# Kernel tuning notes

Measured on AMD Instinct MI355X. Metric: run time of the kernel, lower is better.

## Reference

```python
import jax, jax.numpy as jnp
import numpy as np

B, S, D, H = 4, 2048, 1024, 16
DH = D // H  # 64


def setup_inputs() -> dict:
    key = jax.random.key(0)
    ks = jax.random.split(key, 11)
    s = 0.02
    return {
        "query": jax.random.normal(ks[0], (B, S, D), jnp.float32),
        "key": jax.random.normal(ks[1], (B, S, D), jnp.float32),
        "value": jax.random.normal(ks[2], (B, S, D), jnp.float32),
        "Wq": jax.random.normal(ks[3], (D, D), jnp.float32) * s,
        "bq": jnp.zeros((D,), jnp.float32),
        "Wk": jax.random.normal(ks[4], (D, D), jnp.float32) * s,
        "bk": jnp.zeros((D,), jnp.float32),
        "Wv": jax.random.normal(ks[5], (D, D), jnp.float32) * s,
        "bv": jnp.zeros((D,), jnp.float32),
        "Wo": jax.random.normal(ks[6], (D, D), jnp.float32) * s,
        "bo": jnp.zeros((D,), jnp.float32),
    }


def reference(query, key, value, Wq, bq, Wk, bk, Wv, bv, Wo, bo):
    b, s, _ = query.shape
    # linear projections (torch Linear: x @ W^T + b; here W stored as [in, out])
    q = query @ Wq + bq
    k = key @ Wk + bk
    v = value @ Wv + bv
    # split heads -> [B, H, S, DH]
    q = q.reshape(b, s, H, DH).transpose(0, 2, 1, 3)
    k = k.reshape(b, s, H, DH).transpose(0, 2, 1, 3)
    v = v.reshape(b, s, H, DH).transpose(0, 2, 1, 3)
    scale = jnp.sqrt(jnp.asarray(DH, jnp.float32))
    attn = jnp.einsum("bhqd,bhkd->bhqk", q, k) / scale  # [B,H,S,S]
    attn = jax.nn.softmax(attn, axis=-1)
    out = jnp.einsum("bhqk,bhkd->bhqd", attn, v)
    out = out.transpose(0, 2, 1, 3).reshape(b, s, D)
    return out @ Wo + bo
```

## Files before the change

kernel.cpp:

```cpp
#include <hip/hip_runtime.h>

typedef float f32x4 __attribute__((ext_vector_type(4)));
typedef __bf16 bf16x8 __attribute__((ext_vector_type(8)));
typedef unsigned short u16;
typedef unsigned int u32;
typedef u16 u16x4 __attribute__((ext_vector_type(4)));
typedef u16 u16x8 __attribute__((ext_vector_type(8)));
typedef u32 u32x2 __attribute__((ext_vector_type(2)));
typedef u32 u32x4 __attribute__((ext_vector_type(4)));

constexpr int Bn = 4, Sn = 2048, Dn = 1024, Hn = 16, DHn = 64;
constexpr int Mn = Bn * Sn;

static __device__ __forceinline__ u16 f2bf(float f) {
  return __builtin_bit_cast(u16, (__bf16)f);
}

static __device__ __forceinline__ u32 cvtpk(float lo, float hi) {
  u32 r;
  asm("v_cvt_pk_bf16_f32 %0, %1, %2" : "=v"(r) : "v"(lo), "v"(hi));
  return r;
}

static __device__ __forceinline__ void async16(const void* g, void* l) {
  __builtin_amdgcn_global_load_lds((const __attribute__((address_space(1))) u32*)g,
                                   (__attribute__((address_space(3))) u32*)l, 16, 0, 0);
}

static __device__ __forceinline__ void wait_bar2() {
  asm volatile("s_waitcnt vmcnt(2)" ::: "memory");
  __builtin_amdgcn_sched_barrier(0);
  __builtin_amdgcn_s_barrier();
  __builtin_amdgcn_sched_barrier(0);
}
static __device__ __forceinline__ void wait_bar4() {
  asm volatile("s_waitcnt vmcnt(4)" ::: "memory");
  __builtin_amdgcn_sched_barrier(0);
  __builtin_amdgcn_s_barrier();
  __builtin_amdgcn_sched_barrier(0);
}
static __device__ __forceinline__ void wait_bar8() {
  asm volatile("s_waitcnt vmcnt(8)" ::: "memory");
  __builtin_amdgcn_sched_barrier(0);
  __builtin_amdgcn_s_barrier();
  __builtin_amdgcn_sched_barrier(0);
}
static __device__ __forceinline__ void wait_bar0() {
  asm volatile("s_waitcnt vmcnt(0)" ::: "memory");
  __builtin_amdgcn_sched_barrier(0);
  __builtin_amdgcn_s_barrier();
  __builtin_amdgcn_sched_barrier(0);
}
static __device__ __forceinline__ void raw_bar() {
  __builtin_amdgcn_sched_barrier(0);
  __builtin_amdgcn_s_barrier();
  __builtin_amdgcn_sched_barrier(0);
}
static __device__ __forceinline__ void lgkm_bar() {
  asm volatile("s_waitcnt lgkmcnt(0)" ::: "memory");
  __builtin_amdgcn_sched_barrier(0);
  __builtin_amdgcn_s_barrier();
  __builtin_amdgcn_sched_barrier(0);
}

__global__ void __launch_bounds__(256) transpose4_kernel(const float* __restrict__ Wq,
                                                         const float* __restrict__ Wk,
                                                         const float* __restrict__ Wv,
                                                         const float* __restrict__ Wo,
                                                         u16* __restrict__ Wts) {
  __shared__ float tile[32][33];
  const int z = blockIdx.z;
  const float* W = (z == 0) ? Wq : (z == 1) ? Wk : (z == 2) ? Wv : Wo;
  u16* Wt = Wts + (size_t)z * Dn * Dn;
  const int n0 = blockIdx.x * 32, k0 = blockIdx.y * 32;
  const int tx = threadIdx.x & 31, ty = (threadIdx.x >> 5) * 4;
#pragma unroll
  for (int i = 0; i < 4; ++i)
    tile[ty + i][tx] = W[(size_t)(k0 + ty + i) * Dn + n0 + tx];
  __syncthreads();
#pragma unroll
  for (int i = 0; i < 4; ++i)
    Wt[(size_t)(n0 + ty + i) * Dn + k0 + tx] = f2bf(tile[tx][ty + i]);
}

__global__ void __launch_bounds__(256) gemm_qkv_kernel(const float* __restrict__ q_in,
                                                       const float* __restrict__ k_in,
                                                       const float* __restrict__ v_in,
                                                       const u16* __restrict__ Wts,
                                                       const float* __restrict__ bq,
                                                       const float* __restrict__ bk,
                                                       const float* __restrict__ bv,
                                                       u16* __restrict__ outbase) {
  __shared__ u16 As[2][128 * 64];
  __shared__ u16 Bs[2][128 * 64];

  const int bid = blockIdx.x;
  const int xcd = bid & 7;
  const int loc = bid >> 3;
  const int nb = loc & 7;
  const int panel = xcd * 24 + (loc >> 3);
  const int z = panel >> 6;
  const int m0 = (panel & 63) * 128, n0 = nb * 128;

  const float* A = (z == 0) ? q_in : (z == 1) ? k_in : v_in;
  const u16* Bt = Wts + (size_t)z * Dn * Dn;
  const float* bias = (z == 0) ? bq : (z == 1) ? bk : bv;
  u16* outp = outbase + (size_t)z * Mn * Dn;
  const float scale = (z == 0) ? 0.125f * 1.4426950408889634f : 1.0f;

  const int tid = threadIdx.x;
  const int wave = tid >> 6, lane = tid & 63;
  const int g = lane >> 4, c = lane & 15;
  const int wm = wave >> 1, wn = wave & 1;
  const int srow = lane >> 3, blk = lane & 7;

  f32x4 acc[4][4] = {};
  constexpr int NK = Dn / 64;

  f32x4 ralo[4], rahi[4];

  auto issueA = [&](int k0) {
#pragma unroll
    for (int i = 0; i < 4; ++i) {
      const int row = (wave * 4 + i) * 8 + srow;
      const float* src = A + (size_t)(m0 + row) * Dn + k0 + blk * 8;
      ralo[i] = *(const f32x4*)src;
      rahi[i] = *(const f32x4*)(src + 4);
    }
  };
  auto writeA = [&](u16* dst) {
#pragma unroll
    for (int i = 0; i < 4; ++i) {
      const int row = (wave * 4 + i) * 8 + srow;
      u32x4 w;
      w[0] = cvtpk(ralo[i][0], ralo[i][1]);
      w[1] = cvtpk(ralo[i][2], ralo[i][3]);
      w[2] = cvtpk(rahi[i][0], rahi[i][1]);
      w[3] = cvtpk(rahi[i][2], rahi[i][3]);
      *(u32x4*)(dst + row * 64 + ((blk ^ srow) * 8)) = w;
    }
  };
  auto issueB = [&](int k0, u16* dstB) {
#pragma unroll
    for (int i = 0; i < 4; ++i) {
      const int ch = wave * 4 + i, row = ch * 8 + srow, sb = blk ^ srow;
      async16(Bt + (size_t)(n0 + row) * Dn + k0 + sb * 8, dstB + ch * 512);
    }
  };

  issueA(0);
  issueB(0, Bs[0]);
  asm volatile("s_waitcnt vmcnt(4)" ::: "memory");
  __builtin_amdgcn_sched_barrier(0);
  writeA(As[0]);
  issueA(64);
  issueB(64, Bs[1]);
  asm volatile("s_waitcnt lgkmcnt(0)" ::: "memory");
  __builtin_amdgcn_sched_barrier(0);

  for (int k = 0; k < NK; ++k) {
    const int cur = k & 1;
    if (k + 1 < NK) wait_bar4(); else wait_bar0();

    if (k + 1 < NK) writeA(As[cur ^ 1]);

#pragma unroll
    for (int kk = 0; kk < 2; ++kk) {
      bf16x8 af[4], bfr[4];
#pragma unroll
      for (int mi = 0; mi < 4; ++mi)
        af[mi] = *(const bf16x8*)(As[cur] + (wm * 64 + mi * 16 + c) * 64 +
                                  (((kk * 4 + g) ^ (c & 7)) * 8));
#pragma unroll
      for (int ni = 0; ni < 4; ++ni)
        bfr[ni] = *(const bf16x8*)(Bs[cur] + (wn * 64 + ni * 16 + c) * 64 +
                                   (((kk * 4 + g) ^ (c & 7)) * 8));
#pragma unroll
      for (int mi = 0; mi < 4; ++mi)
#pragma unroll
        for (int ni = 0; ni < 4; ++ni)
          acc[mi][ni] = __builtin_amdgcn_mfma_f32_16x16x32_bf16(af[mi], bfr[ni],
                                                                acc[mi][ni], 0, 0, 0);
    }

    lgkm_bar();
    if (k + 2 < NK) {
      issueA((k + 2) * 64);
      issueB((k + 2) * 64, Bs[cur]);
    }
  }

  const bool vmode = (z == 2);
#pragma unroll
  for (int ni = 0; ni < 4; ++ni) {
    const int col = n0 + wn * 64 + ni * 16 + c;
    const float bv = bias[col];
    const int hh = col >> 6, dh = col & 63;
#pragma unroll
    for (int mi = 0; mi < 4; ++mi) {
      const int row = m0 + wm * 64 + mi * 16 + g * 4;
      const int bb = row >> 11, s = row & 2047;
      if (!vmode) {
        u16* o = outp + (((size_t)(bb * Hn + hh) * Sn + s) * DHn + dh);
#pragma unroll
        for (int r = 0; r < 4; ++r)
          o[(size_t)r * DHn] = f2bf((acc[mi][ni][r] + bv) * scale);
      } else {
        u16x4 pk;
#pragma unroll
        for (int r = 0; r < 4; ++r) pk[r] = f2bf(acc[mi][ni][r] + bv);
        *(u16x4*)(outp + ((size_t)(bb * Hn + hh) * DHn + dh) * Sn + s) = pk;
      }
    }
  }
}

__global__ void __launch_bounds__(256) gemm_o_kernel(const u16* __restrict__ A,
                                                     const u16* __restrict__ Bt,
                                                     const float* __restrict__ bias,
                                                     float* __restrict__ outp) {
  __shared__ u16 As[2][128 * 64];
  __shared__ u16 Bs[2][128 * 64];
  const int bid = blockIdx.x;
  const int xcd = bid & 7;
  const int loc = bid >> 3;
  const int nb = loc & 7;
  const int panel = xcd * 8 + (loc >> 3);
  const int m0 = panel * 128, n0 = nb * 128;

  const int tid = threadIdx.x;
  const int wave = tid >> 6, lane = tid & 63;
  const int g = lane >> 4, c = lane & 15;
  const int wm = wave >> 1, wn = wave & 1;
  const int srow = lane >> 3, blk = lane & 7;

  f32x4 acc[4][4] = {};
  constexpr int NK = Dn / 64;

#pragma unroll
  for (int p = 0; p < 2; ++p) {
    const int k0 = p * 64;
#pragma unroll
    for (int i = 0; i < 4; ++i) {
      const int ch = wave * 4 + i;
      const int row = ch * 8 + srow;
      const int sblk = blk ^ srow;
      async16(A + (size_t)(m0 + row) * Dn + k0 + sblk * 8, As[p] + ch * 512);
      async16(Bt + (size_t)(n0 + row) * Dn + k0 + sblk * 8, Bs[p] + ch * 512);
    }
  }

  for (int k = 0; k < NK; ++k) {
    const int cur = k & 1;
    if (k + 1 < NK) wait_bar8(); else wait_bar0();

#pragma unroll
    for (int kk = 0; kk < 2; ++kk) {
      bf16x8 af[4], bfr[4];
#pragma unroll
      for (int mi = 0; mi < 4; ++mi)
        af[mi] = *(const bf16x8*)(As[cur] + (wm * 64 + mi * 16 + c) * 64 +
                                  (((kk * 4 + g) ^ (c & 7)) * 8));
#pragma unroll
      for (int ni = 0; ni < 4; ++ni)
        bfr[ni] = *(const bf16x8*)(Bs[cur] + (wn * 64 + ni * 16 + c) * 64 +
                                   (((kk * 4 + g) ^ (c & 7)) * 8));
#pragma unroll
      for (int mi = 0; mi < 4; ++mi)
#pragma unroll
        for (int ni = 0; ni < 4; ++ni)
          acc[mi][ni] = __builtin_amdgcn_mfma_f32_16x16x32_bf16(af[mi], bfr[ni],
                                                                acc[mi][ni], 0, 0, 0);
    }

    raw_bar();
    if (k + 2 < NK) {
      const int k0 = (k + 2) * 64;
#pragma unroll
      for (int i = 0; i < 4; ++i) {
        const int ch = wave * 4 + i;
        const int row = ch * 8 + srow;
        const int sblk = blk ^ srow;
        async16(A + (size_t)(m0 + row) * Dn + k0 + sblk * 8, As[cur] + ch * 512);
        async16(Bt + (size_t)(n0 + row) * Dn + k0 + sblk * 8, Bs[cur] + ch * 512);
      }
    }
  }

#pragma unroll
  for (int ni = 0; ni < 4; ++ni) {
    const int col = n0 + wn * 64 + ni * 16 + c;
    const float bv = bias[col];
#pragma unroll
    for (int mi = 0; mi < 4; ++mi) {
      const int row = m0 + wm * 64 + mi * 16 + g * 4;
      float* o = outp + (size_t)row * Dn + col;
#pragma unroll
      for (int r = 0; r < 4; ++r) o[(size_t)r * Dn] = acc[mi][ni][r] + bv;
    }
  }
}

__global__ void __launch_bounds__(512, 4) attn_kernel(const u16* __restrict__ Q,
                                                      const u16* __restrict__ Kp,
                                                      const u16* __restrict__ VT,
                                                      u16* __restrict__ O) {
  __shared__ u16 Ks[3][64 * 64];
  __shared__ u16 Vs[3][64 * 64];
  const int tid = threadIdx.x;
  const int wave = tid >> 6, lane = tid & 63;
  const int g = lane >> 4, c = lane & 15;
  const int bh = blockIdx.x;
  const int q0 = blockIdx.y * 256 + wave * 32;
  const u16* Qb = Q + (size_t)bh * Sn * DHn;
  const u16* Kb = Kp + (size_t)bh * Sn * DHn;
  const u16* Vb = VT + (size_t)bh * DHn * Sn;

  bf16x8 qf[2][2];
#pragma unroll
  for (int fq = 0; fq < 2; ++fq)
#pragma unroll
    for (int kk = 0; kk < 2; ++kk)
      qf[fq][kk] = *(const bf16x8*)(Qb + (size_t)(q0 + fq * 16 + c) * DHn + kk * 32 + g * 8);

  f32x4 ot[4][2] = {};
  f32x4 lacc[2] = {};
  u16x8 one8u;
#pragma unroll
  for (int j = 0; j < 8; ++j) one8u[j] = 0x3F80;
  const bf16x8 one8 = __builtin_bit_cast(bf16x8, one8u);
  const f32x4 zf = {};

  const int srow = lane >> 3, blk = lane & 7;
  const int krow = wave * 8 + srow;
  const int sblk = blk ^ srow;
  constexpr int NT = Sn / 64;

  u16 *kA = Ks[0], *kB = Ks[1], *kC = Ks[2];
  u16 *vA = Vs[0], *vB = Vs[1], *vC = Vs[2];

#pragma unroll
  for (int tt = 0; tt < 2; ++tt) {
    const int kt = tt * 64;
    async16(Kb + (size_t)(kt + krow) * DHn + sblk * 8, Ks[tt] + wave * 512);
    async16(Vb + (size_t)krow * Sn + kt + sblk * 8, Vs[tt] + wave * 512);
  }

  for (int t = 0; t < NT; ++t) {
    if (t + 1 < NT) wait_bar2(); else wait_bar0();

    if (t + 2 < NT) {
      const int kt = (t + 2) * 64;
      async16(Kb + (size_t)(kt + krow) * DHn + sblk * 8, kC + wave * 512);
      async16(Vb + (size_t)krow * Sn + kt + sblk * 8, vC + wave * 512);
    }

    f32x4 st[4][2];
    {
      bf16x8 kf[4];
#pragma unroll
      for (int fk = 0; fk < 4; ++fk)
        kf[fk] = *(const bf16x8*)(kA + (fk * 16 + c) * 64 + ((g ^ (c & 7)) * 8));
      __builtin_amdgcn_s_setprio(1);
#pragma unroll
      for (int fk = 0; fk < 4; ++fk)
#pragma unroll
        for (int fq = 0; fq < 2; ++fq)
          st[fk][fq] = __builtin_amdgcn_mfma_f32_16x16x32_bf16(kf[fk], qf[fq][0],
                                                               zf, 0, 0, 0);
      __builtin_amdgcn_s_setprio(0);
#pragma unroll
      for (int fk = 0; fk < 4; ++fk)
        kf[fk] = *(const bf16x8*)(kA + (fk * 16 + c) * 64 + (((4 + g) ^ (c & 7)) * 8));
      __builtin_amdgcn_s_setprio(1);
#pragma unroll
      for (int fk = 0; fk < 4; ++fk)
#pragma unroll
        for (int fq = 0; fq < 2; ++fq)
          st[fk][fq] = __builtin_amdgcn_mfma_f32_16x16x32_bf16(kf[fk], qf[fq][1],
                                                               st[fk][fq], 0, 0, 0);
      __builtin_amdgcn_s_setprio(0);
    }

#pragma unroll
    for (int fq = 0; fq < 2; ++fq)
#pragma unroll
      for (int fk = 0; fk < 4; ++fk)
#pragma unroll
        for (int r = 0; r < 4; ++r)
          st[fk][fq][r] = __builtin_amdgcn_exp2f(st[fk][fq][r]);

    bf16x8 pf[2][2];
#pragma unroll
    for (int fq = 0; fq < 2; ++fq)
#pragma unroll
      for (int kk = 0; kk < 2; ++kk) {
        u32x4 pw;
#pragma unroll
        for (int w = 0; w < 2; ++w) {
          const u32 a = cvtpk(st[2 * kk][fq][2 * w], st[2 * kk][fq][2 * w + 1]);
          const u32 b = cvtpk(st[2 * kk + 1][fq][2 * w], st[2 * kk + 1][fq][2 * w + 1]);
          const u32x2 p1 = __builtin_amdgcn_permlane32_swap(a, b, false, false);
          const u32x2 p2 = __builtin_amdgcn_permlane16_swap(p1[0], p1[1], false, false);
          pw[w] = p2[0];
          pw[2 + w] = p2[1];
        }
        pf[kk][fq] = __builtin_bit_cast(bf16x8, pw);
      }

#pragma unroll
    for (int kk = 0; kk < 2; ++kk) {
      bf16x8 vf[4];
#pragma unroll
      for (int fa = 0; fa < 4; ++fa)
        vf[fa] = *(const bf16x8*)(vA + (fa * 16 + c) * 64 +
                                  (((kk * 4 + g) ^ (c & 7)) * 8));
      __builtin_amdgcn_s_setprio(1);
#pragma unroll
      for (int fa = 0; fa < 4; ++fa)
#pragma unroll
        for (int fq = 0; fq < 2; ++fq)
          ot[fa][fq] = __builtin_amdgcn_mfma_f32_16x16x32_bf16(vf[fa], pf[kk][fq],
                                                               ot[fa][fq], 0, 0, 0);
#pragma unroll
      for (int fq = 0; fq < 2; ++fq)
        lacc[fq] = __builtin_amdgcn_mfma_f32_16x16x32_bf16(one8, pf[kk][fq],
                                                           lacc[fq], 0, 0, 0);
      __builtin_amdgcn_s_setprio(0);
    }

    u16* tk = kA; kA = kB; kB = kC; kC = tk;
    u16* tv = vA; vA = vB; vB = vC; vC = tv;
  }

  const int bb = bh >> 4, hh = bh & 15;
#pragma unroll
  for (int fq = 0; fq < 2; ++fq) {
    const float inv = 1.f / lacc[fq][0];
    const int s = q0 + fq * 16 + c;
#pragma unroll
    for (int fa = 0; fa < 4; ++fa) {
      const int dh = fa * 16 + g * 4;
      u16x4 pk;
#pragma unroll
      for (int r = 0; r < 4; ++r) pk[r] = f2bf(ot[fa][fq][r] * inv);
      *(u16x4*)(O + ((size_t)bb * Sn + s) * Dn + hh * 64 + dh) = pk;
    }
  }
}

extern "C" void kernel_launch(void* const* d_in, const int* in_sizes, int n_in,
                              void* d_out, int out_size, void* d_ws, size_t ws_size,
                              hipStream_t stream) {
  (void)in_sizes; (void)n_in; (void)out_size; (void)ws_size;
  const float* q_in = (const float*)d_in[0];
  const float* k_in = (const float*)d_in[1];
  const float* v_in = (const float*)d_in[2];
  const float* Wq = (const float*)d_in[3];
  const float* bq = (const float*)d_in[4];
  const float* Wk = (const float*)d_in[5];
  const float* bk = (const float*)d_in[6];
  const float* Wv = (const float*)d_in[7];
  const float* bv = (const float*)d_in[8];
  const float* Wo = (const float*)d_in[9];
  const float* bo = (const float*)d_in[10];

  char* ws = (char*)d_ws;
  const size_t szX = (size_t)Mn * Dn * 2;
  const size_t szW = (size_t)Dn * Dn * 2;
  u16* Wts = (u16*)ws;
  u16* Qb = (u16*)(ws + 4 * szW + 0 * szX);
  u16* Kb = (u16*)(ws + 4 * szW + 1 * szX);
  u16* VTb = (u16*)(ws + 4 * szW + 2 * szX);
  u16* Ob = (u16*)(ws + 4 * szW + 3 * szX);

  transpose4_kernel<<<dim3(32, 32, 4), 256, 0, stream>>>(Wq, Wk, Wv, Wo, Wts);

  gemm_qkv_kernel<<<1536, 256, 0, stream>>>(q_in, k_in, v_in, Wts, bq, bk, bv, Qb);

  attn_kernel<<<dim3(Bn * Hn, Sn / 256), 512, 0, stream>>>(Qb, Kb, VTb, Ob);

  gemm_o_kernel<<<512, 256, 0, stream>>>(Ob, Wts + (size_t)3 * Dn * Dn, bo,
                                         (float*)d_out);
}
```

Before: 180.9 us.

## Pre-convert QKV inputs to bf16 and async-load A tiles into LDS

```diff
diff --git a/kernel.cpp b/kernel.cpp
--- a/kernel.cpp
+++ b/kernel.cpp
@@ -33,12 +33,6 @@
   __builtin_amdgcn_s_barrier();
   __builtin_amdgcn_sched_barrier(0);
 }
-static __device__ __forceinline__ void wait_bar4() {
-  asm volatile("s_waitcnt vmcnt(4)" ::: "memory");
-  __builtin_amdgcn_sched_barrier(0);
-  __builtin_amdgcn_s_barrier();
-  __builtin_amdgcn_sched_barrier(0);
-}
 static __device__ __forceinline__ void wait_bar8() {
   asm volatile("s_waitcnt vmcnt(8)" ::: "memory");
   __builtin_amdgcn_sched_barrier(0);
@@ -56,11 +50,21 @@
   __builtin_amdgcn_s_barrier();
   __builtin_amdgcn_sched_barrier(0);
 }
-static __device__ __forceinline__ void lgkm_bar() {
-  asm volatile("s_waitcnt lgkmcnt(0)" ::: "memory");
-  __builtin_amdgcn_sched_barrier(0);
-  __builtin_amdgcn_s_barrier();
-  __builtin_amdgcn_sched_barrier(0);
+
+__global__ void __launch_bounds__(256) cvt3_kernel(const float* __restrict__ q,
+                                                   const float* __restrict__ k,
+                                                   const float* __restrict__ v,
+                                                   u16* __restrict__ dst) {
+  const int i = blockIdx.x * 256 + threadIdx.x;
+  const int t = i >> 20;
+  const int li = i & 1048575;
+  const float* s = (t == 0) ? q : (t == 1) ? k : v;
+  const f32x4* sp = (const f32x4*)s + (size_t)li * 2;
+  const f32x4 a = sp[0], b = sp[1];
+  u16x8 o;
+  o[0] = f2bf(a[0]); o[1] = f2bf(a[1]); o[2] = f2bf(a[2]); o[3] = f2bf(a[3]);
+  o[4] = f2bf(b[0]); o[5] = f2bf(b[1]); o[6] = f2bf(b[2]); o[7] = f2bf(b[3]);
+  ((u16x8*)dst)[i] = o;
 }
 
 __global__ void __launch_bounds__(256) transpose4_kernel(const float* __restrict__ Wq,
@@ -83,9 +87,7 @@
     Wt[(size_t)(n0 + ty + i) * Dn + k0 + tx] = f2bf(tile[tx][ty + i]);
 }
 
-__global__ void __launch_bounds__(256) gemm_qkv_kernel(const float* __restrict__ q_in,
-                                                       const float* __restrict__ k_in,
-                                                       const float* __restrict__ v_in,
+__global__ void __launch_bounds__(256) gemm_qkv_kernel(const u16* __restrict__ X,
                                                        const u16* __restrict__ Wts,
                                                        const float* __restrict__ bq,
                                                        const float* __restrict__ bk,
@@ -102,7 +104,7 @@
   const int z = panel >> 6;
   const int m0 = (panel & 63) * 128, n0 = nb * 128;
 
-  const float* A = (z == 0) ? q_in : (z == 1) ? k_in : v_in;
+  const u16* A = X + (size_t)z * Mn * Dn;
   const u16* Bt = Wts + (size_t)z * Dn * Dn;
   const float* bias = (z == 0) ? bq : (z == 1) ? bk : bv;
   u16* outp = outbase + (size_t)z * Mn * Dn;
@@ -117,52 +119,22 @@
   f32x4 acc[4][4] = {};
   constexpr int NK = Dn / 64;
 
-  f32x4 ralo[4], rahi[4];
-
-  auto issueA = [&](int k0) {
+#pragma unroll
+  for (int p = 0; p < 2; ++p) {
+    const int k0 = p * 64;
 #pragma unroll
     for (int i = 0; i < 4; ++i) {
-      const int row = (wave * 4 + i) * 8 + srow;
-      const float* src = A + (size_t)(m0 + row) * Dn + k0 + blk * 8;
-      ralo[i] = *(const f32x4*)src;
-      rahi[i] = *(const f32x4*)(src + 4);
-    }
-  };
-  auto writeA = [&](u16* dst) {
-#pragma unroll
-    for (int i = 0; i < 4; ++i) {
-      const int row = (wave * 4 + i) * 8 + srow;
-      u32x4 w;
-      w[0] = cvtpk(ralo[i][0], ralo[i][1]);
-      w[1] = cvtpk(ralo[i][2], ralo[i][3]);
-      w[2] = cvtpk(rahi[i][0], rahi[i][1]);
-      w[3] = cvtpk(rahi[i][2], rahi[i][3]);
-      *(u32x4*)(dst + row * 64 + ((blk ^ srow) * 8)) = w;
-    }
-  };
-  auto issueB = [&](int k0, u16* dstB) {
-#pragma unroll
-    for (int i = 0; i < 4; ++i) {
-      const int ch = wave * 4 + i, row = ch * 8 + srow, sb = blk ^ srow;
-      async16(Bt + (size_t)(n0 + row) * Dn + k0 + sb * 8, dstB + ch * 512);
-    }
-  };
-
-  issueA(0);
-  issueB(0, Bs[0]);
-  asm volatile("s_waitcnt vmcnt(4)" ::: "memory");
-  __builtin_amdgcn_sched_barrier(0);
-  writeA(As[0]);
-  issueA(64);
-  issueB(64, Bs[1]);
-  asm volatile("s_waitcnt lgkmcnt(0)" ::: "memory");
-  __builtin_amdgcn_sched_barrier(0);
+      const int ch = wave * 4 + i;
+      const int row = ch * 8 + srow;
+      const int sblk = blk ^ srow;
+      async16(A + (size_t)(m0 + row) * Dn + k0 + sblk * 8, As[p] + ch * 512);
+      async16(Bt + (size_t)(n0 + row) * Dn + k0 + sblk * 8, Bs[p] + ch * 512);
+    }
+  }
 
   for (int k = 0; k < NK; ++k) {
     const int cur = k & 1;
-    if (k + 1 < NK) wait_bar4(); else wait_bar0();
-
-    if (k + 1 < NK) writeA(As[cur ^ 1]);
+    if (k + 1 < NK) wait_bar8(); else wait_bar0();
 
 #pragma unroll
     for (int kk = 0; kk < 2; ++kk) {
@@ -183,10 +155,17 @@
                                                                 acc[mi][ni], 0, 0, 0);
     }
 
-    lgkm_bar();
+    raw_bar();
     if (k + 2 < NK) {
-      issueA((k + 2) * 64);
-      issueB((k + 2) * 64, Bs[cur]);
+      const int k0 = (k + 2) * 64;
+#pragma unroll
+      for (int i = 0; i < 4; ++i) {
+        const int ch = wave * 4 + i;
+        const int row = ch * 8 + srow;
+        const int sblk = blk ^ srow;
+        async16(A + (size_t)(m0 + row) * Dn + k0 + sblk * 8, As[cur] + ch * 512);
+        async16(Bt + (size_t)(n0 + row) * Dn + k0 + sblk * 8, Bs[cur] + ch * 512);
+      }
     }
   }
 
@@ -468,15 +447,18 @@
   char* ws = (char*)d_ws;
   const size_t szX = (size_t)Mn * Dn * 2;
   const size_t szW = (size_t)Dn * Dn * 2;
-  u16* Wts = (u16*)ws;
-  u16* Qb = (u16*)(ws + 4 * szW + 0 * szX);
-  u16* Kb = (u16*)(ws + 4 * szW + 1 * szX);
-  u16* VTb = (u16*)(ws + 4 * szW + 2 * szX);
-  u16* Ob = (u16*)(ws + 4 * szW + 3 * szX);
+  u16* X = (u16*)ws;
+  u16* Wts = (u16*)(ws + 3 * szX);
+  u16* Qb = (u16*)(ws + 3 * szX + 4 * szW + 0 * szX);
+  u16* Kb = (u16*)(ws + 3 * szX + 4 * szW + 1 * szX);
+  u16* VTb = (u16*)(ws + 3 * szX + 4 * szW + 2 * szX);
+  u16* Ob = (u16*)(ws + 3 * szX + 4 * szW + 3 * szX);
+
+  cvt3_kernel<<<3 * Mn * Dn / 8 / 256, 256, 0, stream>>>(q_in, k_in, v_in, X);
 
   transpose4_kernel<<<dim3(32, 32, 4), 256, 0, stream>>>(Wq, Wk, Wv, Wo, Wts);
 
-  gemm_qkv_kernel<<<1536, 256, 0, stream>>>(q_in, k_in, v_in, Wts, bq, bk, bv, Qb);
+  gemm_qkv_kernel<<<1536, 256, 0, stream>>>(X, Wts, bq, bk, bv, Qb);
 
   attn_kernel<<<dim3(Bn * Hn, Sn / 256), 512, 0, stream>>>(Qb, Kb, VTb, Ob);
 
```

Result: no change. 181.9 us (+0.5%).

## Load QKV GEMM operands straight from global into registers, bypassing LDS

Applied to the files above, without the earlier changes.

```diff
diff --git a/kernel.cpp b/kernel.cpp
--- a/kernel.cpp
+++ b/kernel.cpp
@@ -33,12 +33,6 @@
   __builtin_amdgcn_s_barrier();
   __builtin_amdgcn_sched_barrier(0);
 }
-static __device__ __forceinline__ void wait_bar4() {
-  asm volatile("s_waitcnt vmcnt(4)" ::: "memory");
-  __builtin_amdgcn_sched_barrier(0);
-  __builtin_amdgcn_s_barrier();
-  __builtin_amdgcn_sched_barrier(0);
-}
 static __device__ __forceinline__ void wait_bar8() {
   asm volatile("s_waitcnt vmcnt(8)" ::: "memory");
   __builtin_amdgcn_sched_barrier(0);
@@ -52,12 +46,6 @@
   __builtin_amdgcn_sched_barrier(0);
 }
 static __device__ __forceinline__ void raw_bar() {
-  __builtin_amdgcn_sched_barrier(0);
-  __builtin_amdgcn_s_barrier();
-  __builtin_amdgcn_sched_barrier(0);
-}
-static __device__ __forceinline__ void lgkm_bar() {
-  asm volatile("s_waitcnt lgkmcnt(0)" ::: "memory");
   __builtin_amdgcn_sched_barrier(0);
   __builtin_amdgcn_s_barrier();
   __builtin_amdgcn_sched_barrier(0);
@@ -83,17 +71,14 @@
     Wt[(size_t)(n0 + ty + i) * Dn + k0 + tx] = f2bf(tile[tx][ty + i]);
 }
 
-__global__ void __launch_bounds__(256) gemm_qkv_kernel(const float* __restrict__ q_in,
-                                                       const float* __restrict__ k_in,
-                                                       const float* __restrict__ v_in,
-                                                       const u16* __restrict__ Wts,
-                                                       const float* __restrict__ bq,
-                                                       const float* __restrict__ bk,
-                                                       const float* __restrict__ bv,
-                                                       u16* __restrict__ outbase) {
-  __shared__ u16 As[2][128 * 64];
-  __shared__ u16 Bs[2][128 * 64];
-
+__global__ void __launch_bounds__(256, 2) gemm_qkv_kernel(const float* __restrict__ q_in,
+                                                          const float* __restrict__ k_in,
+                                                          const float* __restrict__ v_in,
+                                                          const u16* __restrict__ Wts,
+                                                          const float* __restrict__ bq,
+                                                          const float* __restrict__ bk,
+                                                          const float* __restrict__ bv,
+                                                          u16* __restrict__ outbase) {
   const int bid = blockIdx.x;
   const int xcd = bid & 7;
   const int loc = bid >> 3;
@@ -112,82 +97,68 @@
   const int wave = tid >> 6, lane = tid & 63;
   const int g = lane >> 4, c = lane & 15;
   const int wm = wave >> 1, wn = wave & 1;
-  const int srow = lane >> 3, blk = lane & 7;
 
   f32x4 acc[4][4] = {};
   constexpr int NK = Dn / 64;
 
-  f32x4 ralo[4], rahi[4];
-
-  auto issueA = [&](int k0) {
-#pragma unroll
-    for (int i = 0; i < 4; ++i) {
-      const int row = (wave * 4 + i) * 8 + srow;
-      const float* src = A + (size_t)(m0 + row) * Dn + k0 + blk * 8;
-      ralo[i] = *(const f32x4*)src;
-      rahi[i] = *(const f32x4*)(src + 4);
-    }
+  const float* Abase = A + (size_t)(m0 + wm * 64 + c) * Dn + g * 8;
+  const u16* Bbase = Bt + (size_t)(n0 + wn * 64 + c) * Dn + g * 8;
+
+  f32x4 a0[4][2][2], a1[4][2][2];
+  bf16x8 b0[4][2], b1[4][2];
+
+  auto loadA = [&](int k0, f32x4 (&a)[4][2][2]) {
+#pragma unroll
+    for (int mi = 0; mi < 4; ++mi)
+#pragma unroll
+      for (int kk = 0; kk < 2; ++kk) {
+        const float* p = Abase + (size_t)(mi * 16) * Dn + k0 + kk * 32;
+        a[mi][kk][0] = *(const f32x4*)p;
+        a[mi][kk][1] = *(const f32x4*)(p + 4);
+      }
   };
-  auto writeA = [&](u16* dst) {
-#pragma unroll
-    for (int i = 0; i < 4; ++i) {
-      const int row = (wave * 4 + i) * 8 + srow;
-      u32x4 w;
-      w[0] = cvtpk(ralo[i][0], ralo[i][1]);
-      w[1] = cvtpk(ralo[i][2], ralo[i][3]);
-      w[2] = cvtpk(rahi[i][0], rahi[i][1]);
-      w[3] = cvtpk(rahi[i][2], rahi[i][3]);
-      *(u32x4*)(dst + row * 64 + ((blk ^ srow) * 8)) = w;
-    }
+  auto loadB = [&](int k0, bf16x8 (&b)[4][2]) {
+#pragma unroll
+    for (int ni = 0; ni < 4; ++ni)
+#pragma unroll
+      for (int kk = 0; kk < 2; ++kk)
+        b[ni][kk] = *(const bf16x8*)(Bbase + (size_t)(ni * 16) * Dn + k0 + kk * 32);
   };
-  auto issueB = [&](int k0, u16* dstB) {
-#pragma unroll
-    for (int i = 0; i < 4; ++i) {
-      const int ch = wave * 4 + i, row = ch * 8 + srow, sb = blk ^ srow;
-      async16(Bt + (size_t)(n0 + row) * Dn + k0 + sb * 8, dstB + ch * 512);
+  auto compute = [&](const f32x4 (&a)[4][2][2], const bf16x8 (&b)[4][2]) {
+#pragma unroll
+    for (int kk = 0; kk < 2; ++kk) {
+      bf16x8 af[4];
+#pragma unroll
+      for (int mi = 0; mi < 4; ++mi) {
+        u32x4 w;
+        w[0] = cvtpk(a[mi][kk][0][0], a[mi][kk][0][1]);
+        w[1] = cvtpk(a[mi][kk][0][2], a[mi][kk][0][3]);
+        w[2] = cvtpk(a[mi][kk][1][0], a[mi][kk][1][1]);
+        w[3] = cvtpk(a[mi][kk][1][2], a[mi][kk][1][3]);
+        af[mi] = __builtin_bit_cast(bf16x8, w);
+      }
+      __builtin_amdgcn_s_setprio(1);
+#pragma unroll
+      for (int mi = 0; mi < 4; ++mi)
+#pragma unroll
+        for (int ni = 0; ni < 4; ++ni)
+          acc[mi][ni] = __builtin_amdgcn_mfma_f32_16x16x32_bf16(af[mi], b[ni][kk],
+                                                                acc[mi][ni], 0, 0, 0);
+      __builtin_amdgcn_s_setprio(0);
     }
   };
 
-  issueA(0);
-  issueB(0, Bs[0]);
-  asm volatile("s_waitcnt vmcnt(4)" ::: "memory");
-  __builtin_amdgcn_sched_barrier(0);
-  writeA(As[0]);
-  issueA(64);
-  issueB(64, Bs[1]);
-  asm volatile("s_waitcnt lgkmcnt(0)" ::: "memory");
-  __builtin_amdgcn_sched_barrier(0);
-
-  for (int k = 0; k < NK; ++k) {
-    const int cur = k & 1;
-    if (k + 1 < NK) wait_bar4(); else wait_bar0();
-
-    if (k + 1 < NK) writeA(As[cur ^ 1]);
-
-#pragma unroll
-    for (int kk = 0; kk < 2; ++kk) {
-      bf16x8 af[4], bfr[4];
-#pragma unroll
-      for (int mi = 0; mi < 4; ++mi)
-        af[mi] = *(const bf16x8*)(As[cur] + (wm * 64 + mi * 16 + c) * 64 +
-                                  (((kk * 4 + g) ^ (c & 7)) * 8));
-#pragma unroll
-      for (int ni = 0; ni < 4; ++ni)
-        bfr[ni] = *(const bf16x8*)(Bs[cur] + (wn * 64 + ni * 16 + c) * 64 +
-                                   (((kk * 4 + g) ^ (c & 7)) * 8));
-#pragma unroll
-      for (int mi = 0; mi < 4; ++mi)
-#pragma unroll
-        for (int ni = 0; ni < 4; ++ni)
-          acc[mi][ni] = __builtin_amdgcn_mfma_f32_16x16x32_bf16(af[mi], bfr[ni],
-                                                                acc[mi][ni], 0, 0, 0);
-    }
-
-    lgkm_bar();
-    if (k + 2 < NK) {
-      issueA((k + 2) * 64);
-      issueB((k + 2) * 64, Bs[cur]);
-    }
+  loadA(0, a0);
+  loadB(0, b0);
+  for (int kp = 0; kp < NK; kp += 2) {
+    loadA((kp + 1) * 64, a1);
+    loadB((kp + 1) * 64, b1);
+    compute(a0, b0);
+    if (kp + 2 < NK) {
+      loadA((kp + 2) * 64, a0);
+      loadB((kp + 2) * 64, b0);
+    }
+    compute(a1, b1);
   }
 
   const bool vmode = (z == 2);
```

Result: slower. 366.3 us (+102.5%).
